# Kernel optimization log

Hardware: AMD Instinct MI355X
Metric: run time of the kernel (lower is better)

The kernel has to match this reference:

```python
import jax, jax.numpy as jnp
import numpy as np

B, T, V, E, D = 64, 512, 512, 128, 256


def setup_inputs() -> dict:
    key = jax.random.key(0)
    ks = jax.random.split(key, 9)
    g = lambda k, sh, s: jax.random.normal(k, sh, jnp.float32) * np.float32(s)
    return {
        "x": jax.random.randint(ks[0], (B, T), 0, V),
        "embed": g(ks[1], (V, E), 1.0),
        "W_ih": g(ks[2], (E, D), 1.0 / np.sqrt(E)),
        "W_hh": g(ks[3], (D, D), 1.0 / np.sqrt(D)),
        "b_h": jnp.zeros((D,), jnp.float32),
        "W_attn": g(ks[4], (D, D), 1.0 / np.sqrt(D)),
        "U_attn": g(ks[5], (D, D), 1.0 / np.sqrt(D)),
        "v_attn": g(ks[6], (D,), 1.0 / np.sqrt(D)),
        "fc_W": g(ks[7], (2 * D, V), 1.0 / np.sqrt(2 * D)),
        "fc_b": jnp.zeros((V,), jnp.float32),
    }


def _forward(x, embed, W_ih, W_hh, b_h, W_attn, U_attn, v_attn, fc_W, fc_b):
    Bn, Tn = x.shape
    Dn = W_hh.shape[0]
    # precompute input projection for every step: [T, B, D]
    xp = jnp.swapaxes(embed[x] @ W_ih + b_h, 0, 1)
    pos = jnp.arange(Tn)

    def step(carry, x_t):
        h_prev, Hbuf, Pbuf, t = carry  # Hbuf: past hidden states, Pbuf: W_attn-projected
        h = jnp.tanh(x_t + h_prev @ W_hh)  # [B, D]
        # Bahdanau attention over strictly-past states (slots < t)
        cur_proj = h @ U_attn  # [B, D]
        energy = jnp.einsum('tbd,d->tb', jnp.tanh(Pbuf + cur_proj[None]), v_attn)
        energy = jnp.where((pos < t)[:, None], energy, -1e9)
        w = jax.nn.softmax(energy, axis=0)  # [T, B]
        ctx = jnp.einsum('tb,tbd->bd', w, Hbuf)
        ctx = jnp.where(t == 0, h, ctx)  # first step: context = h itself
        logits = jnp.concatenate([h, ctx], axis=-1) @ fc_W + fc_b  # [B, V]
        Hbuf = Hbuf.at[t].set(h)
        Pbuf = Pbuf.at[t].set(h @ W_attn)
        return (h, Hbuf, Pbuf, t + 1), logits

    h0 = jnp.zeros((Bn, Dn), xp.dtype)
    buf = jnp.zeros((Tn, Bn, Dn), xp.dtype)
    _, outs = jax.lax.scan(step, (h0, buf, buf, jnp.asarray(0, jnp.int32)), xp)
    return jnp.swapaxes(outs, 0, 1)  # [B, T, V]


def reference(x, embed, W_ih, W_hh, b_h, W_attn, U_attn, v_attn, fc_W, fc_b):
    return _forward(x, embed, W_ih, W_hh, b_h, W_attn, U_attn, v_attn, fc_W, fc_b)
```

## Files before the change

kernel.cpp:

```cpp
#include <hip/hip_runtime.h>
#include <hip/hip_bf16.h>

#define B_  64
#define T_  512
#define V_  512
#define E_  128
#define D_  256
#define D2_ 512

typedef unsigned short u16;
typedef unsigned int   u32;
typedef short s16x8 __attribute__((ext_vector_type(8)));
typedef _Float16 f16x8 __attribute__((ext_vector_type(8)));
typedef float f32x4 __attribute__((ext_vector_type(4)));
typedef unsigned short u16x2 __attribute__((ext_vector_type(2)));
typedef unsigned short u16x4 __attribute__((ext_vector_type(4)));

__device__ __forceinline__ float bf2f(u16 u){
    union { u32 i; float f; } c; c.i = ((u32)u) << 16; return c.f;
}
__device__ __forceinline__ u16 f2bf(float f){
    union { float f; u32 i; } c; c.f = f;
    u32 u = c.i;
    return (u16)((u + 0x7fffu + ((u >> 16) & 1u)) >> 16);
}
__device__ __forceinline__ u16 f2h(float f){
    union { _Float16 h; u16 u; } c; c.h = (_Float16)f; return c.u;
}
__device__ __forceinline__ float tanh_b(float x){
    float e = __expf(2.0f * x);
    return fmaf(-2.0f, __builtin_amdgcn_rcpf(e + 1.0f), 1.0f);
}
__device__ __forceinline__ void barrier_lgkm(){
    asm volatile("s_waitcnt lgkmcnt(0)\n\ts_barrier" ::: "memory");
}

__global__ __launch_bounds__(256) void k_ew(const float* __restrict__ embed,
                                            const float* __restrict__ W_ih,
                                            const float* __restrict__ b_h,
                                            float* __restrict__ EW){
    __shared__ float er[E_];
    int v = blockIdx.x;
    int tid = threadIdx.x;
    if (tid < E_) er[tid] = embed[v*E_ + tid];
    __syncthreads();
    float acc = b_h[tid];
    #pragma unroll 4
    for (int e = 0; e < E_; ++e) acc += er[e] * W_ih[e*D_ + tid];
    EW[v*D_ + tid] = acc;
}

__global__ __launch_bounds__(256) void k_gather(const int* __restrict__ x,
                                                const float* __restrict__ EW,
                                                float* __restrict__ XP){
    int m = blockIdx.x * 4 + (threadIdx.x >> 6);
    int lane = threadIdx.x & 63;
    int b = m & 63, t = m >> 6;
    int v = x[b*T_ + t];
    float4 val = *(const float4*)&EW[v*D_ + lane*4];
    *(float4*)&XP[(size_t)m*D_ + lane*4] = val;
}

__global__ __launch_bounds__(256) void k_cvt(const float* __restrict__ W,
                                             u16* __restrict__ Wb,
                                             int N, int K){
    int i = blockIdx.x * 256 + threadIdx.x;
    int n = i / K, k = i - n*K;
    Wb[(size_t)n*K + k] = f2bf(W[(size_t)k*N + n]);
}

__global__ __launch_bounds__(512, 2) void k_rnn(const float* __restrict__ XP,
                                                const float* __restrict__ W_hh,
                                                u16* __restrict__ HC){
    __shared__ u16 hf[2][4][272];
    int tid  = threadIdx.x;
    int lane = tid & 63;
    int w    = tid >> 6;
    int col  = lane & 15;
    int colA = col & 3;
    int quad = lane >> 4;
    int bb0  = blockIdx.x * 4;

    f16x8 bfh[2][8];
    #pragma unroll
    for (int nt = 0; nt < 2; ++nt){
        int n = w*32 + nt*16 + col;
        #pragma unroll
        for (int ks = 0; ks < 8; ++ks){
            f16x8 th;
            #pragma unroll
            for (int j = 0; j < 8; ++j){
                int k = ks*32 + quad*8 + j;
                th[j] = (_Float16)W_hh[k*D_ + n];
            }
            bfh[nt][ks] = th;
        }
    }
    for (int i = tid; i < 2*4*272; i += 512) (&hf[0][0][0])[i] = 0;

    const float* p  = XP + (size_t)bb0*D_ + w*32 + col;
    u16*         hc = HC + (size_t)bb0*D2_ + w*32 + col;

    float ewv[2][4];
    #pragma unroll
    for (int nt = 0; nt < 2; ++nt)
        #pragma unroll
        for (int r = 0; r < 4; ++r)
            ewv[nt][r] = p[r*D_ + nt*16];
    p += (size_t)B_*D_;
    __syncthreads();

    for (int t = 0; t < T_; ++t){
        int rb = t & 1, wb = rb ^ 1;
        f32x4 acc[2];
        #pragma unroll
        for (int nt = 0; nt < 2; ++nt)
            #pragma unroll
            for (int r = 0; r < 4; ++r) acc[nt][r] = ewv[nt][r];

        f16x8 ah[8];
        #pragma unroll
        for (int ks = 0; ks < 8; ++ks)
            ah[ks] = *(const f16x8*)&hf[rb][colA][ks*32 + quad*8];

        if (t + 1 < T_){
            #pragma unroll
            for (int nt = 0; nt < 2; ++nt)
                #pragma unroll
                for (int r = 0; r < 4; ++r)
                    ewv[nt][r] = p[r*D_ + nt*16];
        }
        p += (size_t)B_*D_;

        #pragma unroll
        for (int ks = 0; ks < 8; ++ks){
            acc[0] = __builtin_amdgcn_mfma_f32_16x16x32_f16(ah[ks], bfh[0][ks], acc[0], 0, 0, 0);
            acc[1] = __builtin_amdgcn_mfma_f32_16x16x32_f16(ah[ks], bfh[1][ks], acc[1], 0, 0, 0);
        }

        #pragma unroll
        for (int nt = 0; nt < 2; ++nt){
            f32x4 s = acc[nt];
            float v = (quad & 2) ? ((quad & 1) ? s[3] : s[2])
                                 : ((quad & 1) ? s[1] : s[0]);
            float h  = tanh_b(v);
            int n    = w*32 + nt*16 + col;
            hf[wb][quad][n]      = f2h(h);
            hc[quad*D2_ + nt*16] = f2bf(h);
        }
        hc += (size_t)B_*D2_;
        barrier_lgkm();
    }
}

__global__ __launch_bounds__(256) void k_gemm(const u16* __restrict__ A, int lda,
                                              const u16* __restrict__ Wb,
                                              const float* __restrict__ bias,
                                              void* __restrict__ out,
                                              int K, int N, int mode){
    __shared__ u16 As[64][88];
    __shared__ u16 Ws[64][88];
    int tid  = threadIdx.x;
    int lane = tid & 63;
    int w    = tid >> 6;
    int col  = lane & 15;
    int quad = lane >> 4;
    int m0   = blockIdx.x * 64;
    int n0   = blockIdx.y * 64;

    f32x4 acc[4];
    #pragma unroll
    for (int nt = 0; nt < 4; ++nt)
        #pragma unroll
        for (int r = 0; r < 4; ++r) acc[nt][r] = 0.0f;

    for (int kk = 0; kk < K; kk += 64){
        #pragma unroll
        for (int i = 0; i < 2; ++i){
            int idx = tid + i*256;
            int r   = idx >> 3;
            int c8  = (idx & 7) * 8;
            *(s16x8*)&As[r][c8] = *(const s16x8*)&A [(size_t)(m0 + r)*lda + kk + c8];
            *(s16x8*)&Ws[r][c8] = *(const s16x8*)&Wb[(size_t)(n0 + r)*K   + kk + c8];
        }
        barrier_lgkm();
        #pragma unroll
        for (int ks = 0; ks < 2; ++ks){
            s16x8 a = *(const s16x8*)&As[w*16 + col][ks*32 + quad*8];
            #pragma unroll
            for (int nt = 0; nt < 4; ++nt){
                s16x8 b = *(const s16x8*)&Ws[nt*16 + col][ks*32 + quad*8];
                acc[nt] = __builtin_amdgcn_mfma_f32_16x16x32_bf16(a, b, acc[nt], 0, 0, 0);
            }
        }
        barrier_lgkm();
    }
    #pragma unroll
    for (int nt = 0; nt < 4; ++nt){
        int n = n0 + nt*16 + col;
        float bv = (mode == 1 && bias) ? bias[n] : 0.0f;
        #pragma unroll
        for (int r = 0; r < 4; ++r){
            int m = m0 + w*16 + quad*4 + r;
            float v = acc[nt][r] + bv;
            if (mode == 1){
                int b = m & 63, t = m >> 6;
                ((float*)out)[(size_t)(b*T_ + t)*V_ + n] = v;
            } else if (mode == 2){
                ((u16*)out)[(size_t)m*N + n] = f2bf(__expf(2.0f * v));
            } else {
                ((u16*)out)[(size_t)m*N + n] = f2bf(v);
            }
        }
    }
}

__global__ __launch_bounds__(256) void k_energy(const u16* __restrict__ EP,
                                                const u16* __restrict__ EQ,
                                                const float* __restrict__ v_attn,
                                                u16* __restrict__ Wx,
                                                float* __restrict__ l){
    __shared__ float eps[32][288];
    int tid = threadIdx.x;
    int blk = blockIdx.x;
    int b   = blk / 136;
    int pi  = blk % 136;
    int tt  = 0;
    while ((tt+1)*(tt+2)/2 <= pi) ++tt;
    int pt  = pi - tt*(tt+1)/2;

    int t_l = tid >> 3;
    int dg  = tid & 7;
    int d0  = dg * 32;
    int t   = tt*32 + t_l;

    #pragma unroll
    for (int i = 0; i < 8; ++i){
        int idx = tid + i*256;
        int row = idx >> 6;
        int c4  = (idx & 63) * 4;
        int pc  = c4 + ((c4 >> 5) << 2);
        u16x4 v4 = *(const u16x4*)&EP[((size_t)((pt*32 + row)*B_ + b))*D_ + c4];
        float4 f4 = make_float4(bf2f(v4.x), bf2f(v4.y), bf2f(v4.z), bf2f(v4.w));
        *(float4*)&eps[row][pc] = f4;
    }

    float eq[32], vm2[32], sv = 0.0f;
    #pragma unroll
    for (int i = 0; i < 8; ++i){
        u16x4 v4 = *(const u16x4*)&EQ[((size_t)(t*B_ + b))*D_ + d0 + i*4];
        eq[i*4+0] = bf2f(v4.x); eq[i*4+1] = bf2f(v4.y);
        eq[i*4+2] = bf2f(v4.z); eq[i*4+3] = bf2f(v4.w);
    }
    #pragma unroll
    for (int i = 0; i < 32; ++i){
        float v = v_attn[d0 + i];
        sv += v;
        vm2[i] = -2.0f * v;
    }
    barrier_lgkm();

    float lsum = 0.0f;
    for (int tpl = 0; tpl < 32; ++tpl){
        int tp = pt*32 + tpl;
        float acc = sv;
        #pragma unroll
        for (int g = 0; g < 8; ++g){
            float4 ep = *(const float4*)&eps[tpl][dg*36 + 4*g];
            float da = fmaf(ep.x, eq[4*g+0], 1.0f);
            float db = fmaf(ep.y, eq[4*g+1], 1.0f);
            float dc = fmaf(ep.z, eq[4*g+2], 1.0f);
            float dd = fmaf(ep.w, eq[4*g+3], 1.0f);
            float dab = da * db;
            float dcd = dc * dd;
            float nab = fmaf(vm2[4*g+1], da, vm2[4*g+0] * db);
            float ncd = fmaf(vm2[4*g+3], dc, vm2[4*g+2] * dd);
            float num = fmaf(ncd, dab, nab * dcd);
            acc = fmaf(num, __builtin_amdgcn_rcpf(dab * dcd), acc);
        }
        acc += __shfl_xor(acc, 1);
        acc += __shfl_xor(acc, 2);
        acc += __shfl_xor(acc, 4);
        float pe = __expf(acc);
        if (dg == 0 && tp < t){
            u16 peb = f2bf(pe);
            Wx[((size_t)(b*T_ + t))*T_ + tp] = peb;
            lsum += bf2f(peb);
        }
    }
    if (dg == 0 && lsum != 0.0f) atomicAdd(&l[b*T_ + t], lsum);
}

__global__ __launch_bounds__(256) void k_ctx(const u16* __restrict__ Wx,
                                             u16* __restrict__ HC,
                                             const float* __restrict__ l){
    __shared__ u16 As[64][88];
    __shared__ u16 Ws[64][88];
    int tid  = threadIdx.x;
    int lane = tid & 63;
    int w    = tid >> 6;
    int col  = lane & 15;
    int quad = lane >> 4;
    int b    = blockIdx.y;
    int m0   = (blockIdx.x >> 2) * 64;
    int n0   = (blockIdx.x & 3) * 64;

    const u16* A = Wx + (size_t)b * T_ * T_;

    f32x4 acc[4];
    #pragma unroll
    for (int nt = 0; nt < 4; ++nt)
        #pragma unroll
        for (int r = 0; r < 4; ++r) acc[nt][r] = 0.0f;

    for (int kk = 0; kk < T_; kk += 64){
        #pragma unroll
        for (int i = 0; i < 2; ++i){
            int idx = tid + i*256;
            int r   = idx >> 3;
            int c8  = (idx & 7) * 8;
            *(s16x8*)&As[r][c8] = *(const s16x8*)&A[(size_t)(m0 + r)*T_ + kk + c8];
        }
        #pragma unroll
        for (int i = 0; i < 8; ++i){
            int idx = tid + i*256;
            int k   = idx >> 5;
            int n2  = (idx & 31) * 2;
            u16x2 v2 = *(const u16x2*)&HC[((size_t)((kk + k)*B_ + b))*D2_ + n0 + n2];
            Ws[n2][k]   = v2.x;
            Ws[n2+1][k] = v2.y;
        }
        barrier_lgkm();
        #pragma unroll
        for (int ks = 0; ks < 2; ++ks){
            s16x8 a = *(const s16x8*)&As[w*16 + col][ks*32 + quad*8];
            #pragma unroll
            for (int nt = 0; nt < 4; ++nt){
                s16x8 bb = *(const s16x8*)&Ws[nt*16 + col][ks*32 + quad*8];
                acc[nt] = __builtin_amdgcn_mfma_f32_16x16x32_bf16(a, bb, acc[nt], 0, 0, 0);
            }
        }
        barrier_lgkm();
    }

    float linv[4];
    #pragma unroll
    for (int r = 0; r < 4; ++r){
        int t = m0 + w*16 + quad*4 + r;
        float lv = (t > 0) ? l[b*T_ + t] : 1.0f;
        linv[r] = 1.0f / lv;
    }
    #pragma unroll
    for (int nt = 0; nt < 4; ++nt){
        int n = n0 + nt*16 + col;
        #pragma unroll
        for (int r = 0; r < 4; ++r){
            int t = m0 + w*16 + quad*4 + r;
            u16 ov;
            if (t == 0) ov = HC[(size_t)b*D2_ + n];
            else        ov = f2bf(acc[nt][r] * linv[r]);
            HC[((size_t)(t*B_ + b))*D2_ + D_ + n] = ov;
        }
    }
}

extern "C" void kernel_launch(void* const* d_in, const int* in_sizes, int n_in,
                              void* d_out, int out_size, void* d_ws, size_t ws_size,
                              hipStream_t stream){
    const int*   x     = (const int*)d_in[0];
    const float* embed = (const float*)d_in[1];
    const float* W_ih  = (const float*)d_in[2];
    const float* W_hh  = (const float*)d_in[3];
    const float* b_h   = (const float*)d_in[4];
    const float* W_att = (const float*)d_in[5];
    const float* U_att = (const float*)d_in[6];
    const float* v_att = (const float*)d_in[7];
    const float* fc_W  = (const float*)d_in[8];
    const float* fc_b  = (const float*)d_in[9];

    char* ws = (char*)d_ws;
    float* EW   = (float*)ws;
    u16*   fcWb = (u16*)ws;
    u16*   HC   = (u16*)(ws + 524288);
    u16*   EP   = (u16*)(ws + 34078720);
    u16*   EQ   = (u16*)(ws + 50855936);
    float* XP   = (float*)(ws + 34078720);
    float* l    = (float*)(ws + 67633152);
    u16*   Wab  = (u16*)(ws + 67764224);
    u16*   Uab  = (u16*)(ws + 67895296);
    u16*   Wx   = (u16*)d_out;

    hipMemsetAsync(d_out, 0, (size_t)B_*T_*T_*2, stream);
    hipMemsetAsync(l, 0, B_*T_*4, stream);

    k_ew    <<<dim3(V_),          dim3(256), 0, stream>>>(embed, W_ih, b_h, EW);
    k_gather<<<dim3(T_*B_/4),     dim3(256), 0, stream>>>(x, EW, XP);
    k_cvt   <<<dim3(D_*D_/256),   dim3(256), 0, stream>>>(W_att, Wab, D_, D_);
    k_cvt   <<<dim3(D_*D_/256),   dim3(256), 0, stream>>>(U_att, Uab, D_, D_);
    k_cvt   <<<dim3(D2_*V_/256),  dim3(256), 0, stream>>>(fc_W, fcWb, V_, D2_);
    k_rnn   <<<dim3(16),          dim3(512), 0, stream>>>(XP, W_hh, HC);
    k_gemm  <<<dim3(512, 4),      dim3(256), 0, stream>>>(HC, D2_, Wab, nullptr, (void*)EP, D_, D_, 2);
    k_gemm  <<<dim3(512, 4),      dim3(256), 0, stream>>>(HC, D2_, Uab, nullptr, (void*)EQ, D_, D_, 2);
    k_energy<<<dim3(B_*136),      dim3(256), 0, stream>>>(EP, EQ, v_att, Wx, l);
    k_ctx   <<<dim3(32, B_),      dim3(256), 0, stream>>>(Wx, HC, l);
    k_gemm  <<<dim3(512, 8),      dim3(256), 0, stream>>>(HC, D2_, fcWb, fc_b, d_out, D2_, V_, 1);
}
```

Measured before the change: 731.0 us.

## Merge attention projection GEMMs, add 128x128 FC kernel, skip masked context tiles

The two separate W_attn and U_attn projection GEMMs become one launch with N=512. A new output mode splits the results into the EP and EQ buffers, which relies on Wab/Uab and EP/EQ sitting contiguously in the workspace. The final FC projection moves to a dedicated 512-thread kernel with 128x128 tiles for better operand reuse. The context GEMM now stops its K loop at the causal boundary, skipping attention-weight tiles that are zero anyway.

```diff
diff --git a/kernel.cpp b/kernel.cpp
--- a/kernel.cpp
+++ b/kernel.cpp
@@ -208,8 +208,74 @@
                 ((float*)out)[(size_t)(b*T_ + t)*V_ + n] = v;
             } else if (mode == 2){
                 ((u16*)out)[(size_t)m*N + n] = f2bf(__expf(2.0f * v));
+            } else if (mode == 3){
+                u16* dst = (u16*)out + ((size_t)(n >> 8)) * ((size_t)32768 * 256);
+                dst[(size_t)m*256 + (n & 255)] = f2bf(__expf(2.0f * v));
             } else {
                 ((u16*)out)[(size_t)m*N + n] = f2bf(v);
+            }
+        }
+    }
+}
+
+__global__ __launch_bounds__(512) void k_fc(const u16* __restrict__ A,
+                                            const u16* __restrict__ Wb,
+                                            const float* __restrict__ bias,
+                                            float* __restrict__ out){
+    __shared__ u16 As[128][88];
+    __shared__ u16 Ws[128][88];
+    int tid  = threadIdx.x;
+    int lane = tid & 63;
+    int w    = tid >> 6;
+    int wm   = w >> 2;
+    int wn   = w & 3;
+    int col  = lane & 15;
+    int quad = lane >> 4;
+    int m0   = blockIdx.x * 128;
+    int n0   = blockIdx.y * 128;
+
+    f32x4 acc[4][2];
+    #pragma unroll
+    for (int mt = 0; mt < 4; ++mt)
+        #pragma unroll
+        for (int nt = 0; nt < 2; ++nt)
+            #pragma unroll
+            for (int r = 0; r < 4; ++r) acc[mt][nt][r] = 0.0f;
+
+    for (int kk = 0; kk < D2_; kk += 64){
+        #pragma unroll
+        for (int i = 0; i < 2; ++i){
+            int idx = tid + i*512;
+            int r   = idx >> 3;
+            int c8  = (idx & 7) * 8;
+            *(s16x8*)&As[r][c8] = *(const s16x8*)&A [(size_t)(m0 + r)*D2_ + kk + c8];
+            *(s16x8*)&Ws[r][c8] = *(const s16x8*)&Wb[(size_t)(n0 + r)*D2_ + kk + c8];
+        }
+        barrier_lgkm();
+        #pragma unroll
+        for (int ks = 0; ks < 2; ++ks){
+            s16x8 b0 = *(const s16x8*)&Ws[wn*32 +      col][ks*32 + quad*8];
+            s16x8 b1 = *(const s16x8*)&Ws[wn*32 + 16 + col][ks*32 + quad*8];
+            #pragma unroll
+            for (int mt = 0; mt < 4; ++mt){
+                s16x8 a = *(const s16x8*)&As[wm*64 + mt*16 + col][ks*32 + quad*8];
+                acc[mt][0] = __builtin_amdgcn_mfma_f32_16x16x32_bf16(a, b0, acc[mt][0], 0, 0, 0);
+                acc[mt][1] = __builtin_amdgcn_mfma_f32_16x16x32_bf16(a, b1, acc[mt][1], 0, 0, 0);
+            }
+        }
+        barrier_lgkm();
+    }
+    #pragma unroll
+    for (int nt = 0; nt < 2; ++nt){
+        int n = n0 + wn*32 + nt*16 + col;
+        float bv = bias[n];
+        #pragma unroll
+        for (int mt = 0; mt < 4; ++mt){
+            #pragma unroll
+            for (int r = 0; r < 4; ++r){
+                int m = m0 + wm*64 + mt*16 + quad*4 + r;
+                int b = m & 63, t = m >> 6;
+                out[(size_t)(b*T_ + t)*V_ + n] = acc[mt][nt][r] + bv;
             }
         }
     }
@@ -313,7 +379,8 @@
         #pragma unroll
         for (int r = 0; r < 4; ++r) acc[nt][r] = 0.0f;
 
-    for (int kk = 0; kk < T_; kk += 64){
+    int kmax = m0 + 64;
+    for (int kk = 0; kk < kmax; kk += 64){
         #pragma unroll
         for (int i = 0; i < 2; ++i){
             int idx = tid + i*256;
@@ -390,8 +457,8 @@
     u16*   Uab  = (u16*)(ws + 67895296);
     u16*   Wx   = (u16*)d_out;
 
-    hipMemsetAsync(d_out, 0, (size_t)B_*T_*T_*2, stream);
-    hipMemsetAsync(l, 0, B_*T_*4, stream);
+    (void)hipMemsetAsync(d_out, 0, (size_t)B_*T_*T_*2, stream);
+    (void)hipMemsetAsync(l, 0, B_*T_*4, stream);
 
     k_ew    <<<dim3(V_),          dim3(256), 0, stream>>>(embed, W_ih, b_h, EW);
     k_gather<<<dim3(T_*B_/4),     dim3(256), 0, stream>>>(x, EW, XP);
@@ -399,9 +466,8 @@
     k_cvt   <<<dim3(D_*D_/256),   dim3(256), 0, stream>>>(U_att, Uab, D_, D_);
     k_cvt   <<<dim3(D2_*V_/256),  dim3(256), 0, stream>>>(fc_W, fcWb, V_, D2_);
     k_rnn   <<<dim3(16),          dim3(512), 0, stream>>>(XP, W_hh, HC);
-    k_gemm  <<<dim3(512, 4),      dim3(256), 0, stream>>>(HC, D2_, Wab, nullptr, (void*)EP, D_, D_, 2);
-    k_gemm  <<<dim3(512, 4),      dim3(256), 0, stream>>>(HC, D2_, Uab, nullptr, (void*)EQ, D_, D_, 2);
+    k_gemm  <<<dim3(512, 8),      dim3(256), 0, stream>>>(HC, D2_, Wab, nullptr, (void*)EP, D_, D2_, 3);
     k_energy<<<dim3(B_*136),      dim3(256), 0, stream>>>(EP, EQ, v_att, Wx, l);
     k_ctx   <<<dim3(32, B_),      dim3(256), 0, stream>>>(Wx, HC, l);
-    k_gemm  <<<dim3(512, 8),      dim3(256), 0, stream>>>(HC, D2_, fcWb, fc_b, d_out, D2_, V_, 1);
-}
+    k_fc    <<<dim3(256, 4),      dim3(512), 0, stream>>>(HC, fcWb, fc_b, (float*)d_out);
+}
```

New measurement: 702.7 us. 1.04x faster.
